# Optimization experiments

Measured on AMD Instinct MI355X. Metric: run time of the kernel, lower is better.

Reference implementation:

```python
import jax, jax.numpy as jnp
import numpy as np

HIDDEN = 4096
N_HEADS = 32
N_KV_HEADS = 8
HEAD_DIM = HIDDEN // N_HEADS  # 128
B, S = 2, 4096


def setup_inputs() -> dict:
    key = jax.random.key(0)
    ks = jax.random.split(key, 9)
    sc = 1.0 / np.sqrt(HIDDEN)
    x = jax.random.normal(ks[0], (B, S, HIDDEN), dtype=jnp.float32)
    Wq = jax.random.normal(ks[1], (HIDDEN, HIDDEN), dtype=jnp.float32) * sc
    bq = jax.random.normal(ks[2], (HIDDEN,), dtype=jnp.float32) * 0.01
    Wk = jax.random.normal(ks[3], (N_KV_HEADS * HEAD_DIM, HIDDEN), dtype=jnp.float32) * sc
    bk = jax.random.normal(ks[4], (N_KV_HEADS * HEAD_DIM,), dtype=jnp.float32) * 0.01
    Wv = jax.random.normal(ks[5], (N_KV_HEADS * HEAD_DIM, HIDDEN), dtype=jnp.float32) * sc
    bv = jax.random.normal(ks[6], (N_KV_HEADS * HEAD_DIM,), dtype=jnp.float32) * 0.01
    Wo = jax.random.normal(ks[7], (HIDDEN, HIDDEN), dtype=jnp.float32) * sc
    bo = jax.random.normal(ks[8], (HIDDEN,), dtype=jnp.float32) * 0.01
    return {"x": x, "Wq": Wq, "bq": bq, "Wk": Wk, "bk": bk,
            "Wv": Wv, "bv": bv, "Wo": Wo, "bo": bo}


def reference(x, Wq, bq, Wk, bk, Wv, bv, Wo, bo):
    batch, seq, _ = x.shape
    # Linear projections (torch Linear: x @ W^T + b)
    q = x @ Wq.T + bq                      # [B,S,H*D]
    k = x @ Wk.T + bk                      # [B,S,Hkv*D]
    v = x @ Wv.T + bv
    q = q.reshape(batch, seq, N_HEADS, HEAD_DIM)
    k = k.reshape(batch, seq, N_KV_HEADS, HEAD_DIM)
    v = v.reshape(batch, seq, N_KV_HEADS, HEAD_DIM)
    # GQA handling in source: concatenate [k]*r along head axis (a TILE, not interleave)
    r = N_HEADS // N_KV_HEADS
    k = jnp.tile(k, (1, 1, r, 1))          # [B,S,H,D]
    v = jnp.tile(v, (1, 1, r, 1))
    # Source keeps layout [B,S,H,D]; mx.matmul batches over (B,S), so
    # attention is taken ACROSS THE HEAD AXIS per token (faithful to source).
    scores = jnp.einsum('bshd,bsgd->bshg', q, k) / np.sqrt(HEAD_DIM)  # [B,S,H,H]
    weights = jax.nn.softmax(scores, axis=-1)
    attn = jnp.einsum('bshg,bsgd->bshd', weights, v)  # [B,S,H,D]
    attn = attn.reshape(batch, seq, HIDDEN)
    return attn @ Wo.T + bo
```

## Files before the change

kernel.cpp:

```cpp
#include <hip/hip_runtime.h>
#include <hip/hip_bf16.h>


typedef _Float16 half8 __attribute__((ext_vector_type(8)));
typedef _Float16 half4v __attribute__((ext_vector_type(4)));
typedef float floatx16 __attribute__((ext_vector_type(16)));

#define K_DIM 4096
#define LDAB 8192
#define BM 256
#define BN 256
#define BK 32
#define NSTEP 128

__device__ __forceinline__ void gload16(const void* g, void* l) {
    __builtin_amdgcn_global_load_lds((const __attribute__((address_space(1))) void*)g,
                                     (__attribute__((address_space(3))) void*)l,
                                     16, 0, 0);
}

__global__ __launch_bounds__(256) void split_f32(
    const float* __restrict__ src, _Float16* __restrict__ dst, long long rows) {
    long long n4 = rows * 1024;
    long long stride = (long long)gridDim.x * blockDim.x;
    for (long long i = (long long)blockIdx.x * blockDim.x + threadIdx.x; i < n4; i += stride) {
        float4 v = ((const float4*)src)[i];
        long long r = i >> 10;
        int c = ((int)(i & 1023)) << 2;
        half4v hi, lo;
        hi[0] = (_Float16)v.x; lo[0] = (_Float16)(v.x - (float)hi[0]);
        hi[1] = (_Float16)v.y; lo[1] = (_Float16)(v.y - (float)hi[1]);
        hi[2] = (_Float16)v.z; lo[2] = (_Float16)(v.z - (float)hi[2]);
        hi[3] = (_Float16)v.w; lo[3] = (_Float16)(v.w - (float)hi[3]);
        *(half4v*)&dst[r * LDAB + c] = hi;
        *(half4v*)&dst[r * LDAB + K_DIM + c] = lo;
    }
}

__global__ __launch_bounds__(512, 2) void gemm_split3_8w(
    const _Float16* __restrict__ A, const _Float16* __restrict__ B,
    float* __restrict__ C, const float* __restrict__ bias0,
    const float* __restrict__ bias1, int N) {

    __shared__ __attribute__((aligned(16))) _Float16 lA[2][2][BM * BK];
    __shared__ __attribute__((aligned(16))) _Float16 lB[2][2][BN * BK];

    const int tid = threadIdx.x;
    const int lane = tid & 63;
    const int w = tid >> 6;
    const int wm = w >> 2;
    const int wn = w & 3;

    const int f = blockIdx.x;
    const int nwg = gridDim.x;
    const int lid = (f & 7) * (nwg >> 3) + (f >> 3);
    const long long brow = (long long)(lid & 31) * BM;
    const long long bcol = (long long)(lid >> 5) * BN;

    floatx16 acc[4][2];
#pragma unroll
    for (int m = 0; m < 4; ++m)
#pragma unroll
        for (int n = 0; n < 2; ++n)
            acc[m][n] = (floatx16)(0.f);

    const int srow = w * 16 + (lane >> 2);
    const int scol = 8 * ((lane & 3) ^ ((lane >> 3) & 3));
    const _Float16* Asrc = A + (brow + srow) * (long long)LDAB + scol;
    const _Float16* Bsrc = B + (bcol + srow) * (long long)LDAB + scol;

    const int rl = lane & 31;
    const int rbase8 = ((rl >> 4) * 64 + (rl & 15) * 4) * 8;
    const int x0 = (((lane >> 5) ^ ((lane >> 1) & 3))) * 8;
    const int x1 = (((2 + (lane >> 5)) ^ ((lane >> 1) & 3))) * 8;

    auto stageG1 = [&](int NXT, int ktn) {
        gload16(Asrc + ktn, &lA[NXT][0][w * 512]);
        gload16(Asrc + 128 * (long long)LDAB + ktn, &lA[NXT][0][4096 + w * 512]);
        gload16(Bsrc + ktn, &lB[NXT][0][w * 512]);
        gload16(Bsrc + 128 * (long long)LDAB + ktn, &lB[NXT][0][4096 + w * 512]);
    };
    auto stageG23 = [&](int NXT, int ktn) {
        gload16(Bsrc + K_DIM + ktn, &lB[NXT][1][w * 512]);
        gload16(Bsrc + 128 * (long long)LDAB + K_DIM + ktn, &lB[NXT][1][4096 + w * 512]);
        gload16(Asrc + K_DIM + ktn, &lA[NXT][1][w * 512]);
        gload16(Asrc + 128 * (long long)LDAB + K_DIM + ktn, &lA[NXT][1][4096 + w * 512]);
    };

    stageG1(0, 0);
    stageG23(0, 0);

    auto step = [&](int CUR, int NXT, int ktn) {
        half8 ah[4][2], bh[2][2];
        asm volatile("s_waitcnt vmcnt(4)" ::: "memory");
        __builtin_amdgcn_s_barrier();
#pragma unroll
        for (int nf = 0; nf < 2; ++nf) {
            bh[nf][0] = *(const half8*)&lB[CUR][0][(wn * 4 + nf * 2) * 512 + rbase8 + x0];
            bh[nf][1] = *(const half8*)&lB[CUR][0][(wn * 4 + nf * 2) * 512 + rbase8 + x1];
        }
#pragma unroll
        for (int mf = 0; mf < 4; ++mf) {
            ah[mf][0] = *(const half8*)&lA[CUR][0][(wm * 8 + mf * 2) * 512 + rbase8 + x0];
            ah[mf][1] = *(const half8*)&lA[CUR][0][(wm * 8 + mf * 2) * 512 + rbase8 + x1];
        }
        stageG1(NXT, ktn);
        __builtin_amdgcn_s_setprio(1);
#pragma unroll
        for (int mf = 0; mf < 4; ++mf)
#pragma unroll
            for (int nf = 0; nf < 2; ++nf) {
                acc[mf][nf] = __builtin_amdgcn_mfma_f32_32x32x16_f16(
                    ah[mf][0], bh[nf][0], acc[mf][nf], 0, 0, 0);
                acc[mf][nf] = __builtin_amdgcn_mfma_f32_32x32x16_f16(
                    ah[mf][1], bh[nf][1], acc[mf][nf], 0, 0, 0);
            }
        __builtin_amdgcn_s_setprio(0);
        asm volatile("s_waitcnt vmcnt(4)" ::: "memory");
        __builtin_amdgcn_s_barrier();
        {
            half8 bl[2][2];
#pragma unroll
            for (int nf = 0; nf < 2; ++nf) {
                bl[nf][0] = *(const half8*)&lB[CUR][1][(wn * 4 + nf * 2) * 512 + rbase8 + x0];
                bl[nf][1] = *(const half8*)&lB[CUR][1][(wn * 4 + nf * 2) * 512 + rbase8 + x1];
            }
            stageG23(NXT, ktn);
            __builtin_amdgcn_s_setprio(1);
#pragma unroll
            for (int mf = 0; mf < 4; ++mf)
#pragma unroll
                for (int nf = 0; nf < 2; ++nf) {
                    acc[mf][nf] = __builtin_amdgcn_mfma_f32_32x32x16_f16(
                        ah[mf][0], bl[nf][0], acc[mf][nf], 0, 0, 0);
                    acc[mf][nf] = __builtin_amdgcn_mfma_f32_32x32x16_f16(
                        ah[mf][1], bl[nf][1], acc[mf][nf], 0, 0, 0);
                }
            __builtin_amdgcn_s_setprio(0);
        }
        {
            half8 al[4][2];
#pragma unroll
            for (int mf = 0; mf < 4; ++mf) {
                al[mf][0] = *(const half8*)&lA[CUR][1][(wm * 8 + mf * 2) * 512 + rbase8 + x0];
                al[mf][1] = *(const half8*)&lA[CUR][1][(wm * 8 + mf * 2) * 512 + rbase8 + x1];
            }
            __builtin_amdgcn_s_setprio(1);
#pragma unroll
            for (int mf = 0; mf < 4; ++mf)
#pragma unroll
                for (int nf = 0; nf < 2; ++nf) {
                    acc[mf][nf] = __builtin_amdgcn_mfma_f32_32x32x16_f16(
                        al[mf][0], bh[nf][0], acc[mf][nf], 0, 0, 0);
                    acc[mf][nf] = __builtin_amdgcn_mfma_f32_32x32x16_f16(
                        al[mf][1], bh[nf][1], acc[mf][nf], 0, 0, 0);
                }
            __builtin_amdgcn_s_setprio(0);
        }
    };

    for (int tt = 0; tt < NSTEP; tt += 2) {
        step(0, 1, (tt + 1) * BK);
        step(1, 0, ((tt + 2) & (NSTEP - 1)) * BK);
    }
    asm volatile("s_waitcnt vmcnt(0)" ::: "memory");

    const float* bias = (bias1 != nullptr && bcol >= 1024) ? (bias1 - 1024) : bias0;
    const int r0 = 4 * (lane >> 5);
#pragma unroll
    for (int nf = 0; nf < 2; ++nf) {
        long long col = bcol + wn * 64 + nf * 32 + rl;
        float bv_ = bias[col];
#pragma unroll
        for (int mf = 0; mf < 4; ++mf) {
            long long rowb = brow + wm * 128 + mf * 32 + r0;
#pragma unroll
            for (int g = 0; g < 4; ++g)
#pragma unroll
                for (int rr = 0; rr < 4; ++rr) {
                    long long row = rowb + 8 * g + rr;
                    __builtin_nontemporal_store(acc[mf][nf][g * 4 + rr] + bv_,
                                                C + row * (long long)N + col);
                }
        }
    }
}

__global__ __launch_bounds__(256) void attn_token(
    const float* __restrict__ q, const float* __restrict__ kv,
    _Float16* __restrict__ out) {

    const int token = blockIdx.x;
    __shared__ float sQ[32 * 128];
    __shared__ float sK[8 * 128];
    __shared__ float sV[8 * 128];
    __shared__ float sP[32 * 8];

    const int t = threadIdx.x;
    {
        const float4* gq = (const float4*)(q + (long long)token * 4096);
        float4* dq = (float4*)sQ;
        dq[t] = gq[t];
        dq[t + 256] = gq[t + 256];
        dq[t + 512] = gq[t + 512];
        dq[t + 768] = gq[t + 768];
        const float4* gkv = (const float4*)(kv + (long long)token * 2048);
        ((float4*)sK)[t] = gkv[t];
        ((float4*)sV)[t] = gkv[t + 256];
    }
    __syncthreads();

    const int h = t >> 3, j = t & 7;
    const float* qr = sQ + h * 128;
    const float* kr = sK + j * 128;
    float s = 0.f;
#pragma unroll
    for (int i = 0; i < 128; i += 4)
        s += qr[i] * kr[i] + qr[i + 1] * kr[i + 1] +
             qr[i + 2] * kr[i + 2] + qr[i + 3] * kr[i + 3];
    s *= 0.08838834764831845f;

    float mx = s;
    mx = fmaxf(mx, __shfl_xor(mx, 1, 8));
    mx = fmaxf(mx, __shfl_xor(mx, 2, 8));
    mx = fmaxf(mx, __shfl_xor(mx, 4, 8));
    float e = expf(s - mx);
    float sum = e;
    sum += __shfl_xor(sum, 1, 8);
    sum += __shfl_xor(sum, 2, 8);
    sum += __shfl_xor(sum, 4, 8);
    sP[t] = e / sum;
    __syncthreads();

    float p[8];
#pragma unroll
    for (int jj = 0; jj < 8; ++jj) p[jj] = sP[(t >> 3) * 8 + jj];
    const int d0 = (t & 7) * 16;
    const long long obase = (long long)token * LDAB + (t >> 3) * 128;
#pragma unroll
    for (int dd = 0; dd < 16; ++dd) {
        int d = d0 + dd;
        float a = 0.f;
#pragma unroll
        for (int jj = 0; jj < 8; ++jj) a += p[jj] * sV[jj * 128 + d];
        _Float16 hi = (_Float16)a;
        _Float16 lo = (_Float16)(a - (float)hi);
        out[obase + d] = hi;
        out[obase + K_DIM + d] = lo;
    }
}

extern "C" void kernel_launch(void* const* d_in, const int* in_sizes, int n_in,
                              void* d_out, int out_size, void* d_ws, size_t ws_size,
                              hipStream_t stream) {
    const float* x  = (const float*)d_in[0];
    const float* Wq = (const float*)d_in[1];
    const float* bq = (const float*)d_in[2];
    const float* Wk = (const float*)d_in[3];
    const float* bk = (const float*)d_in[4];
    const float* Wv = (const float*)d_in[5];
    const float* bv = (const float*)d_in[6];
    const float* Wo = (const float*)d_in[7];
    const float* bo = (const float*)d_in[8];
    float* out = (float*)d_out;

    char* ws = (char*)d_ws;
    _Float16* A2x  = (_Float16*)(ws + 0);
    _Float16* B2q  = (_Float16*)(ws + 134217728LL);
    _Float16* B2kv = (_Float16*)(ws + 201326592LL);
    _Float16* B2v  = (_Float16*)(ws + 218103808LL);
    _Float16* B2o  = (_Float16*)(ws + 234881024LL);
    float*    qb   = (float*)(ws + 301989888LL);
    float*    kvb  = (float*)(ws + 436207616LL);

    split_f32<<<2048, 256, 0, stream>>>(x,  A2x, 8192);
    split_f32<<<2048, 256, 0, stream>>>(Wq, B2q, 4096);
    split_f32<<<1024, 256, 0, stream>>>(Wk, B2kv, 1024);
    split_f32<<<1024, 256, 0, stream>>>(Wv, B2v, 1024);
    split_f32<<<2048, 256, 0, stream>>>(Wo, B2o, 4096);

    gemm_split3_8w<<<512, 512, 0, stream>>>(A2x, B2q,  qb,  bq, nullptr, 4096);
    gemm_split3_8w<<<256, 512, 0, stream>>>(A2x, B2kv, kvb, bk, bv,      2048);

    attn_token<<<8192, 256, 0, stream>>>(qb, kvb, A2x);

    gemm_split3_8w<<<512, 512, 0, stream>>>(A2x, B2o, out, bo, nullptr, 4096);
}
```

Measured before the change: 2.583 ms.

## Stage GEMM tiles in MFMA-fragment order so LDS reads are linear

Changes the global-to-LDS staging so each wave loads 32 rows by 8 halves per 16-byte lane directly in the register-fragment order the 32x32x16 MFMA expects. Fragment reads from LDS then become a simple lane*8 offset instead of the swizzled rbase/x0/x1 addressing. This removes the XOR swizzle arithmetic and aims for conflict-free, contiguous ds_read_b128. The trade-off is that the global loads are less coalesced: each lane now reads 16 bytes from a different row.

Result: slower. 2.951 ms (+14.3%).

```diff
diff --git a/kernel.cpp b/kernel.cpp
--- a/kernel.cpp
+++ b/kernel.cpp
@@ -42,8 +42,8 @@
     float* __restrict__ C, const float* __restrict__ bias0,
     const float* __restrict__ bias1, int N) {
 
-    __shared__ __attribute__((aligned(16))) _Float16 lA[2][2][BM * BK];
-    __shared__ __attribute__((aligned(16))) _Float16 lB[2][2][BN * BK];
+    __shared__ __attribute__((aligned(16))) _Float16 lA[2][2][8192];
+    __shared__ __attribute__((aligned(16))) _Float16 lB[2][2][8192];
 
     const int tid = threadIdx.x;
     const int lane = tid & 63;
@@ -64,27 +64,24 @@
         for (int n = 0; n < 2; ++n)
             acc[m][n] = (floatx16)(0.f);
 
-    const int srow = w * 16 + (lane >> 2);
-    const int scol = 8 * ((lane & 3) ^ ((lane >> 3) & 3));
-    const _Float16* Asrc = A + (brow + srow) * (long long)LDAB + scol;
-    const _Float16* Bsrc = B + (bcol + srow) * (long long)LDAB + scol;
-
-    const int rl = lane & 31;
-    const int rbase8 = ((rl >> 4) * 64 + (rl & 15) * 4) * 8;
-    const int x0 = (((lane >> 5) ^ ((lane >> 1) & 3))) * 8;
-    const int x1 = (((2 + (lane >> 5)) ^ ((lane >> 1) & 3))) * 8;
+    const _Float16* Asrc = A + (brow + w * 32 + (lane & 31)) * (long long)LDAB
+                             + ((lane >> 5) << 3);
+    const _Float16* Bsrc = B + (bcol + w * 32 + (lane & 31)) * (long long)LDAB
+                             + ((lane >> 5) << 3);
+
+    const int rfo = lane * 8;
 
     auto stageG1 = [&](int NXT, int ktn) {
-        gload16(Asrc + ktn, &lA[NXT][0][w * 512]);
-        gload16(Asrc + 128 * (long long)LDAB + ktn, &lA[NXT][0][4096 + w * 512]);
-        gload16(Bsrc + ktn, &lB[NXT][0][w * 512]);
-        gload16(Bsrc + 128 * (long long)LDAB + ktn, &lB[NXT][0][4096 + w * 512]);
+        gload16(Asrc + ktn,      &lA[NXT][0][(w * 2 + 0) * 512]);
+        gload16(Asrc + ktn + 16, &lA[NXT][0][(w * 2 + 1) * 512]);
+        gload16(Bsrc + ktn,      &lB[NXT][0][(w * 2 + 0) * 512]);
+        gload16(Bsrc + ktn + 16, &lB[NXT][0][(w * 2 + 1) * 512]);
     };
     auto stageG23 = [&](int NXT, int ktn) {
-        gload16(Bsrc + K_DIM + ktn, &lB[NXT][1][w * 512]);
-        gload16(Bsrc + 128 * (long long)LDAB + K_DIM + ktn, &lB[NXT][1][4096 + w * 512]);
-        gload16(Asrc + K_DIM + ktn, &lA[NXT][1][w * 512]);
-        gload16(Asrc + 128 * (long long)LDAB + K_DIM + ktn, &lA[NXT][1][4096 + w * 512]);
+        gload16(Bsrc + K_DIM + ktn,      &lB[NXT][1][(w * 2 + 0) * 512]);
+        gload16(Bsrc + K_DIM + ktn + 16, &lB[NXT][1][(w * 2 + 1) * 512]);
+        gload16(Asrc + K_DIM + ktn,      &lA[NXT][1][(w * 2 + 0) * 512]);
+        gload16(Asrc + K_DIM + ktn + 16, &lA[NXT][1][(w * 2 + 1) * 512]);
     };
 
     stageG1(0, 0);
@@ -95,15 +92,15 @@
         asm volatile("s_waitcnt vmcnt(4)" ::: "memory");
         __builtin_amdgcn_s_barrier();
 #pragma unroll
-        for (int nf = 0; nf < 2; ++nf) {
-            bh[nf][0] = *(const half8*)&lB[CUR][0][(wn * 4 + nf * 2) * 512 + rbase8 + x0];
-            bh[nf][1] = *(const half8*)&lB[CUR][0][(wn * 4 + nf * 2) * 512 + rbase8 + x1];
-        }
-#pragma unroll
-        for (int mf = 0; mf < 4; ++mf) {
-            ah[mf][0] = *(const half8*)&lA[CUR][0][(wm * 8 + mf * 2) * 512 + rbase8 + x0];
-            ah[mf][1] = *(const half8*)&lA[CUR][0][(wm * 8 + mf * 2) * 512 + rbase8 + x1];
-        }
+        for (int nf = 0; nf < 2; ++nf)
+#pragma unroll
+            for (int x = 0; x < 2; ++x)
+                bh[nf][x] = *(const half8*)&lB[CUR][0][((wn * 2 + nf) * 2 + x) * 512 + rfo];
+#pragma unroll
+        for (int mf = 0; mf < 4; ++mf)
+#pragma unroll
+            for (int x = 0; x < 2; ++x)
+                ah[mf][x] = *(const half8*)&lA[CUR][0][((wm * 4 + mf) * 2 + x) * 512 + rfo];
         stageG1(NXT, ktn);
         __builtin_amdgcn_s_setprio(1);
 #pragma unroll
@@ -121,10 +118,10 @@
         {
             half8 bl[2][2];
 #pragma unroll
-            for (int nf = 0; nf < 2; ++nf) {
-                bl[nf][0] = *(const half8*)&lB[CUR][1][(wn * 4 + nf * 2) * 512 + rbase8 + x0];
-                bl[nf][1] = *(const half8*)&lB[CUR][1][(wn * 4 + nf * 2) * 512 + rbase8 + x1];
-            }
+            for (int nf = 0; nf < 2; ++nf)
+#pragma unroll
+                for (int x = 0; x < 2; ++x)
+                    bl[nf][x] = *(const half8*)&lB[CUR][1][((wn * 2 + nf) * 2 + x) * 512 + rfo];
             stageG23(NXT, ktn);
             __builtin_amdgcn_s_setprio(1);
 #pragma unroll
@@ -141,10 +138,10 @@
         {
             half8 al[4][2];
 #pragma unroll
-            for (int mf = 0; mf < 4; ++mf) {
-                al[mf][0] = *(const half8*)&lA[CUR][1][(wm * 8 + mf * 2) * 512 + rbase8 + x0];
-                al[mf][1] = *(const half8*)&lA[CUR][1][(wm * 8 + mf * 2) * 512 + rbase8 + x1];
-            }
+            for (int mf = 0; mf < 4; ++mf)
+#pragma unroll
+                for (int x = 0; x < 2; ++x)
+                    al[mf][x] = *(const half8*)&lA[CUR][1][((wm * 4 + mf) * 2 + x) * 512 + rfo];
             __builtin_amdgcn_s_setprio(1);
 #pragma unroll
             for (int mf = 0; mf < 4; ++mf)
@@ -166,6 +163,7 @@
     asm volatile("s_waitcnt vmcnt(0)" ::: "memory");
 
     const float* bias = (bias1 != nullptr && bcol >= 1024) ? (bias1 - 1024) : bias0;
+    const int rl = lane & 31;
     const int r0 = 4 * (lane >> 5);
 #pragma unroll
     for (int nf = 0; nf < 2; ++nf) {
```
